# Performance work log

Measured on AMD Instinct MI355X. Metric: run time of the kernel, lower is better.

The kernel has to match this reference:

```python
import jax, jax.numpy as jnp
import numpy as np

B, S, H = 4, 2048, 1024
NH, HD = 16, 64
LN_EPS = 1e-5


def _l2norm(x, axis=-1, eps=1e-12):
    n = jnp.sqrt(jnp.sum(x * x, axis=axis, keepdims=True))
    return x / jnp.maximum(n, eps)


def setup_inputs() -> dict:
    key = jax.random.key(0)
    ks = jax.random.split(key, 10)
    sd = 0.02
    x = jax.random.normal(ks[0], (B, S, H), jnp.float32)
    Wq = jax.random.normal(ks[1], (H, H), jnp.float32) * sd
    Wk = jax.random.normal(ks[2], (H, H), jnp.float32) * sd
    Wv = jax.random.normal(ks[3], (H, H), jnp.float32) * sd
    Wa = jax.random.normal(ks[4], (NH, H), jnp.float32) * sd
    ba = jnp.zeros((NH,), jnp.float32)
    Wb = jax.random.normal(ks[5], (NH, H), jnp.float32) * sd
    bb = jnp.zeros((NH,), jnp.float32)
    Wg = jax.random.normal(ks[6], (H, H), jnp.float32) * sd
    Wo = jax.random.normal(ks[7], (H, H), jnp.float32) * sd
    ln_g = jnp.ones((H,), jnp.float32)
    ln_b = jnp.zeros((H,), jnp.float32)
    return {"x": x, "Wq": Wq, "Wk": Wk, "Wv": Wv, "Wa": Wa, "ba": ba,
            "Wb": Wb, "bb": bb, "Wg": Wg, "Wo": Wo, "ln_g": ln_g, "ln_b": ln_b}


def _forward(x, Wq, Wk, Wv, Wa, ba, Wb, bb, Wg, Wo, ln_g, ln_b):
    q = _l2norm((x @ Wq.T).reshape(B, S, NH, HD))  # [B,S,nh,hd]
    k = _l2norm((x @ Wk.T).reshape(B, S, NH, HD))
    v = jax.nn.silu(x @ Wv.T).reshape(B, S, NH, HD)
    alpha = jax.nn.sigmoid(x @ Wa.T + ba)  # [B,S,nh]
    beta = jax.nn.sigmoid(x @ Wb.T + bb)   # [B,S,nh]

    def step(state, inp):
        a_t, b_t, k_t, v_t, q_t = inp  # a,b: [B,nh]; k,v,q: [B,nh,hd]
        a_ = a_t[:, :, None, None]
        b_ = b_t[:, :, None, None]
        kk = k_t[..., :, None] * k_t[..., None, :]  # [B,nh,hd,hd]
        state = a_ * state * (1.0 - b_ * kk) + b_ * (v_t[..., :, None] * k_t[..., None, :])
        out_t = jnp.sum(state * q_t[..., None, :], axis=-1)  # [B,nh,hd]
        return state, out_t

    # time-major xs for scan
    xs = (jnp.moveaxis(alpha, 1, 0), jnp.moveaxis(beta, 1, 0),
          jnp.moveaxis(k, 1, 0), jnp.moveaxis(v, 1, 0), jnp.moveaxis(q, 1, 0))
    state0 = jnp.zeros((B, NH, HD, HD), x.dtype)
    _, outs = jax.lax.scan(step, state0, xs)  # [S,B,nh,hd]
    out = jnp.moveaxis(outs, 0, 1).reshape(B, S, H)

    # LayerNorm over total_dim
    mu = jnp.mean(out, axis=-1, keepdims=True)
    var = jnp.var(out, axis=-1, keepdims=True)
    out = (out - mu) / jnp.sqrt(var + LN_EPS) * ln_g + ln_b

    out = out * jax.nn.silu(x @ Wg.T)
    return out @ Wo.T


def reference(x, Wq, Wk, Wv, Wa, ba, Wb, bb, Wg, Wo, ln_g, ln_b):
    return _forward(x, Wq, Wk, Wv, Wa, ba, Wb, bb, Wg, Wo, ln_g, ln_b)
```

## Files before the change

kernel.cpp:

```cpp
#include <hip/hip_runtime.h>

typedef unsigned short u16;
typedef __bf16 bf16x8 __attribute__((ext_vector_type(8)));
typedef float f32x4 __attribute__((ext_vector_type(4)));

constexpr int Bq  = 4;
constexpr int Sq  = 2048;
constexpr int Hq  = 1024;
constexpr int NHq = 16;
constexpr int HDq = 64;
constexpr int CCH = 16;
constexpr int LCH = 128;

constexpr size_t OFF_WB = 0;
constexpr size_t OFF_XB = 10485760;
constexpr size_t OFF_Q  = 27262976;
constexpr size_t OFF_K  = 60817408;
constexpr size_t OFF_V  = 94371840;
constexpr size_t OFF_G  = 127926272;
constexpr size_t OFF_AL = 161480704;
constexpr size_t OFF_BE = 162004992;
constexpr size_t OFF_P  = 162529280;
constexpr size_t OFF_O  = 179306496;

__device__ __forceinline__ u16 f2bf(float f) {
  unsigned u = __float_as_uint(f);
  u += 0x7fffu + ((u >> 16) & 1u);
  return (u16)(u >> 16);
}
__device__ __forceinline__ float sigmoidf_(float x) { return 1.f / (1.f + __expf(-x)); }

__device__ __forceinline__ void async16(const void* g, void* l) {
  __builtin_amdgcn_global_load_lds((const __attribute__((address_space(1))) void*)g,
                                   (__attribute__((address_space(3))) void*)l, 16, 0, 0);
}

__global__ __launch_bounds__(256) void cvt_x_kernel(const float* __restrict__ in, u16* __restrict__ outp) {
  const size_t i = ((size_t)blockIdx.x * 256 + threadIdx.x) * 4;
  float4 f = *(const float4*)(in + i);
  ushort4 u; u.x = f2bf(f.x); u.y = f2bf(f.y); u.z = f2bf(f.z); u.w = f2bf(f.w);
  *(ushort4*)(outp + i) = u;
}

__global__ __launch_bounds__(256) void cvt_w_kernel(const float* __restrict__ w0, const float* __restrict__ w1,
    const float* __restrict__ w2, const float* __restrict__ w3, const float* __restrict__ w4,
    u16* __restrict__ outp) {
  const int z = blockIdx.z;
  const float* src = (z == 0) ? w0 : (z == 1) ? w1 : (z == 2) ? w2 : (z == 3) ? w3 : w4;
  const size_t i = ((size_t)blockIdx.x * 256 + threadIdx.x) * 4;
  float4 f = *(const float4*)(src + i);
  ushort4 u; u.x = f2bf(f.x); u.y = f2bf(f.y); u.z = f2bf(f.z); u.w = f2bf(f.w);
  *(ushort4*)(outp + (size_t)z * (1024 * 1024) + i) = u;
}

__global__ __launch_bounds__(256) void cvt_ab_kernel(const float* __restrict__ Wa, const float* __restrict__ Wb,
    u16* __restrict__ outp) {
  const size_t i = ((size_t)blockIdx.x * 256 + threadIdx.x) * 4;
  const int row = (int)(i >> 10);
  ushort4 u;
  if (row < 32) {
    const float* src = (row < 16) ? (Wa + i) : (Wb + i - 16 * 1024);
    float4 f = *(const float4*)src;
    u.x = f2bf(f.x); u.y = f2bf(f.y); u.z = f2bf(f.z); u.w = f2bf(f.w);
  } else {
    u.x = u.y = u.z = u.w = 0;
  }
  *(ushort4*)(outp + i) = u;
}


__device__ __forceinline__ void lda4(bf16x8 af[4][2], const u16* LA, int wr, int mh, int l15, int qd, int l7) {
#pragma unroll
  for (int i = 0; i < 4; ++i)
#pragma unroll
    for (int kk = 0; kk < 2; ++kk)
      af[i][kk] = *(const bf16x8*)(LA + (wr * 128 + mh * 64 + i * 16 + l15) * 64 + (((kk * 4 + qd) ^ l7) * 8));
}
__device__ __forceinline__ void ldb2(bf16x8 bf[2][2], const u16* LB, int wc, int nh, int l15, int qd, int l7) {
#pragma unroll
  for (int j = 0; j < 2; ++j)
#pragma unroll
    for (int kk = 0; kk < 2; ++kk)
      bf[j][kk] = *(const bf16x8*)(LB + (wc * 64 + nh * 32 + j * 16 + l15) * 64 + (((kk * 4 + qd) ^ l7) * 8));
}
__device__ __forceinline__ void mm16(f32x4 acc[8][4], const bf16x8 af[4][2], const bf16x8 bf[2][2], int mh, int nh) {
#pragma unroll
  for (int i = 0; i < 4; ++i)
#pragma unroll
    for (int j = 0; j < 2; ++j) {
      f32x4 c = acc[mh * 4 + i][nh * 2 + j];
      c = __builtin_amdgcn_mfma_f32_16x16x32_bf16(af[i][0], bf[j][0], c, 0, 0, 0);
      c = __builtin_amdgcn_mfma_f32_16x16x32_bf16(af[i][1], bf[j][1], c, 0, 0, 0);
      acc[mh * 4 + i][nh * 2 + j] = c;
    }
}
__device__ __forceinline__ void stageH(u16* LD, int bufp, int mat, int h, const u16* gRow0, int kElem,
                                       int rr, int sl8, int wv) {
  const u16* s0 = gRow0 + (size_t)(h * 128 + rr) * 1024 + kElem + sl8;
  u16* d = LD + bufp * 32768 + mat * 16384 + h * 8192 + wv * 512;
  async16(s0, d);
  async16(s0 + (size_t)(64 * 1024), d + 4096);
}

template<int S1, int S2, int VM>
__device__ __forceinline__ void tile16(u16* LD, int bp, int kt,
    const u16* gA, const u16* gB, f32x4 acc[8][4], bf16x8 af[4][2], bf16x8 bf0[2][2], bf16x8 bf1[2][2],
    int wr, int wc, int l15, int qd, int l7, int rr, int sl8, int wv) {
  const u16* LA = LD + bp * 32768;
  const u16* LB = LA + 16384;
  lda4(af, LA, wr, 0, l15, qd, l7);
  ldb2(bf0, LB, wc, 0, l15, qd, l7);
  if (S1) stageH(LD, bp ^ 1, 0, 0, gA, (kt + 1) * 64, rr, sl8, wv);
  __builtin_amdgcn_s_barrier();
  asm volatile("s_waitcnt lgkmcnt(0)" ::: "memory");
  __builtin_amdgcn_sched_barrier(0);
  __builtin_amdgcn_s_setprio(1);
  mm16(acc, af, bf0, 0, 0);
  __builtin_amdgcn_s_setprio(0);
  __builtin_amdgcn_s_barrier();
  ldb2(bf1, LB, wc, 1, l15, qd, l7);
  if (S1) stageH(LD, bp ^ 1, 0, 1, gA, (kt + 1) * 64, rr, sl8, wv);
  __builtin_amdgcn_s_barrier();
  asm volatile("s_waitcnt lgkmcnt(0)" ::: "memory");
  __builtin_amdgcn_sched_barrier(0);
  __builtin_amdgcn_s_setprio(1);
  mm16(acc, af, bf1, 0, 1);
  __builtin_amdgcn_s_setprio(0);
  __builtin_amdgcn_s_barrier();
  lda4(af, LA, wr, 1, l15, qd, l7);
  if (S2) stageH(LD, bp, 1, 0, gB, (kt + 2) * 64, rr, sl8, wv);
  __builtin_amdgcn_s_barrier();
  asm volatile("s_waitcnt lgkmcnt(0)" ::: "memory");
  __builtin_amdgcn_sched_barrier(0);
  __builtin_amdgcn_s_setprio(1);
  mm16(acc, af, bf0, 1, 0);
  __builtin_amdgcn_s_setprio(0);
  __builtin_amdgcn_s_barrier();
  if (S2) stageH(LD, bp, 1, 1, gB, (kt + 2) * 64, rr, sl8, wv);
  __builtin_amdgcn_s_barrier();
  __builtin_amdgcn_sched_barrier(0);
  __builtin_amdgcn_s_setprio(1);
  mm16(acc, af, bf1, 1, 1);
  __builtin_amdgcn_s_setprio(0);
  if (VM == 4) asm volatile("s_waitcnt vmcnt(4)" ::: "memory");
  else if (VM == 0) asm volatile("s_waitcnt vmcnt(0)" ::: "memory");
  __builtin_amdgcn_s_barrier();
}

__global__ __launch_bounds__(512, 2) void gemm256(const u16* __restrict__ A, const u16* __restrict__ Wall,
    const u16* __restrict__ Wab,
    float* __restrict__ Cq, float* __restrict__ Ck, float* __restrict__ Cv, float* __restrict__ Cg,
    float* __restrict__ al, float* __restrict__ be,
    const float* __restrict__ ba, const float* __restrict__ bb, int mode) {
  __shared__ __align__(16) u16 Lds[65536];
  u16* LD = &Lds[0];
  const int tid = threadIdx.x;
  const int wv = tid >> 6, lane = tid & 63;
  const int l15 = lane & 15, qd = lane >> 4, l7 = l15 & 7;
  const int wr = wv >> 2, wc = wv & 3;
  const int rr = tid >> 3, sl8 = ((tid & 7) ^ (rr & 7)) * 8;

  int mx, ny, z;
  const u16* Wm;
  if (mode == 0) { mx = blockIdx.x & 31; ny = blockIdx.x >> 5; z = 0; Wm = Wall; }
  else if (blockIdx.x < 32) { mx = blockIdx.x; ny = 0; z = 4; Wm = Wab; }
  else {
    const int b = blockIdx.x - 32;
    mx = b & 31; ny = (b >> 5) & 3; z = b >> 7;
    Wm = Wall + (size_t)z * (1024 * 1024);
  }
  const int m0 = mx * 256, n0 = ny * 256;
  const u16* gA = A + (size_t)m0 * 1024;
  const u16* gB = Wm + (size_t)n0 * 1024;

  f32x4 acc[8][4] = {};
  bf16x8 af[4][2], bf0[2][2], bf1[2][2];

  stageH(LD, 0, 0, 0, gA, 0,  rr, sl8, wv);
  stageH(LD, 0, 0, 1, gA, 0,  rr, sl8, wv);
  stageH(LD, 0, 1, 0, gB, 0,  rr, sl8, wv);
  stageH(LD, 0, 1, 1, gB, 0,  rr, sl8, wv);
  stageH(LD, 1, 1, 0, gB, 64, rr, sl8, wv);
  stageH(LD, 1, 1, 1, gB, 64, rr, sl8, wv);
  asm volatile("s_waitcnt vmcnt(4)" ::: "memory");
  __builtin_amdgcn_s_barrier();

#pragma unroll 1
  for (int t2 = 0; t2 < 7; ++t2) {
    tile16<1, 1, 4>(LD, 0, 2 * t2,     gA, gB, acc, af, bf0, bf1, wr, wc, l15, qd, l7, rr, sl8, wv);
    tile16<1, 1, 4>(LD, 1, 2 * t2 + 1, gA, gB, acc, af, bf0, bf1, wr, wc, l15, qd, l7, rr, sl8, wv);
  }
  tile16<1, 0, 0>(LD, 0, 14, gA, gB, acc, af, bf0, bf1, wr, wc, l15, qd, l7, rr, sl8, wv);
  tile16<0, 0, -1>(LD, 1, 15, gA, gB, acc, af, bf0, bf1, wr, wc, l15, qd, l7, rr, sl8, wv);

  if (mode == 1 && z == 4) {
    if (wc == 0) {
      const float bav = ba[l15], bbv = bb[l15];
#pragma unroll
      for (int mi = 0; mi < 8; ++mi) {
        const int row = m0 + wr * 128 + mi * 16 + qd * 4;
#pragma unroll
        for (int r = 0; r < 4; ++r) {
          al[(size_t)(row + r) * 16 + l15] = sigmoidf_(acc[mi][0][r] + bav);
          be[(size_t)(row + r) * 16 + l15] = sigmoidf_(acc[mi][1][r] + bbv);
        }
      }
    }
    return;
  }
  if (mode == 1 && z <= 1) {
#pragma unroll
    for (int mi = 0; mi < 8; ++mi)
#pragma unroll
      for (int r = 0; r < 4; ++r) {
        float ss = acc[mi][0][r] * acc[mi][0][r] + acc[mi][1][r] * acc[mi][1][r]
                 + acc[mi][2][r] * acc[mi][2][r] + acc[mi][3][r] * acc[mi][3][r];
        ss += __shfl_xor(ss, 1); ss += __shfl_xor(ss, 2);
        ss += __shfl_xor(ss, 4); ss += __shfl_xor(ss, 8);
        const float rn = 1.f / fmaxf(sqrtf(ss), 1e-12f);
        acc[mi][0][r] *= rn; acc[mi][1][r] *= rn; acc[mi][2][r] *= rn; acc[mi][3][r] *= rn;
      }
  } else if (mode == 1 && z == 2) {
#pragma unroll
    for (int mi = 0; mi < 8; ++mi)
#pragma unroll
      for (int ni = 0; ni < 4; ++ni)
#pragma unroll
        for (int r = 0; r < 4; ++r)
          acc[mi][ni][r] = acc[mi][ni][r] * sigmoidf_(acc[mi][ni][r]);
  }
  float* C = (mode == 0) ? Cq : ((z == 0) ? Cq : (z == 1) ? Ck : (z == 2) ? Cv : Cg);
#pragma unroll
  for (int mi = 0; mi < 8; ++mi) {
    const int row = m0 + wr * 128 + mi * 16 + qd * 4;
#pragma unroll
    for (int ni = 0; ni < 4; ++ni) {
      const int col = n0 + wc * 64 + ni * 16 + l15;
#pragma unroll
      for (int r = 0; r < 4; ++r)
        C[(size_t)(row + r) * 1024 + col] = acc[mi][ni][r];
    }
  }
}

struct ScanLds1 { float kb[2][2][16 * 64]; float vb[2][2][16 * 64]; float ab[2][2][32]; };
struct ScanLds2 { float kb[2][2][16 * 64]; float qb[2][2][16 * 64]; float vb[2][2][16 * 64]; float ab[2][2][32]; };

__global__ __launch_bounds__(256, 2) void scan_p1(const float* __restrict__ k, const float* __restrict__ v,
    const float* __restrict__ al, const float* __restrict__ be,
    float* __restrict__ P, float* __restrict__ Q) {
  __shared__ ScanLds1 L;
  const int tid = threadIdx.x, wv = tid >> 6, lane = tid & 63;
  const int bh = blockIdx.x >> 3, cp = blockIdx.x & 7;
  const int b = bh >> 4, h = bh & 15;
  const int cw = wv >> 1, half = wv & 1;
  const int c = cp * 2 + cw;
  const int rg = lane >> 3, cg = lane & 7;
  const int r0 = half * 32 + rg * 4, c8 = cg * 8;
  const size_t base0[2] = { ((size_t)(b * Sq + (cp * 2 + 0) * LCH)) * 1024 + h * 64,
                            ((size_t)(b * Sq + (cp * 2 + 1) * LCH)) * 1024 + h * 64 };
  const size_t ab0[2]   = { ((size_t)(b * Sq + (cp * 2 + 0) * LCH)) * 16 + h,
                            ((size_t)(b * Sq + (cp * 2 + 1) * LCH)) * 16 + h };
  const int tokw = lane >> 4, seg = lane & 15;
  auto stage = [&](int tile, int bi) {
    #pragma unroll
    for (int j = 0; j < 4; ++j) {
      const int job = wv * 4 + j;
      const int ch = job >> 3, rem = job & 7, arr = rem >> 2, i = rem & 3;
      const float* src = arr ? v : k;
      float* dst = arr ? &L.vb[bi][ch][i * 256] : &L.kb[bi][ch][i * 256];
      async16(src + base0[ch] + (size_t)(tile * 16 + i * 4 + tokw) * 1024 + seg * 4, dst);
    }
    if (wv == 0) {
      const int ch = lane >> 5, w16 = (lane >> 4) & 1, tt = lane & 15;
      const float* s = w16 ? be : al;
      L.ab[bi][ch][w16 * 16 + tt] = s[ab0[ch] + (size_t)(tile * 16 + tt) * 16];
    }
  };
  float Pr[32], Qr[32];
  #pragma unroll
  for (int i = 0; i < 32; ++i) { Pr[i] = 1.f; Qr[i] = 0.f; }
  stage(0, 0);
  for (int tile = 0; tile < 8; ++tile) {
    __syncthreads();
    if (tile < 7) stage(tile + 1, (tile + 1) & 1);
    const int bi = tile & 1;
    const float* kbp = L.kb[bi][cw];
    const float* vbp = L.vb[bi][cw];
    const float* abp = L.ab[bi][cw];
    #pragma unroll 2
    for (int tt = 0; tt < 16; ++tt) {
      const float a = abp[tt], bt = abp[16 + tt];
      float4 kcv0 = *(const float4*)(kbp + tt * 64 + c8);
      float4 kcv1 = *(const float4*)(kbp + tt * 64 + c8 + 4);
      float4 krvv = *(const float4*)(kbp + tt * 64 + r0);
      float4 vrvv = *(const float4*)(vbp + tt * 64 + r0);
      const float kcv[8] = {kcv0.x, kcv0.y, kcv0.z, kcv0.w, kcv1.x, kcv1.y, kcv1.z, kcv1.w};
      const float krv[4] = {krvv.x, krvv.y, krvv.z, krvv.w};
      const float vrv[4] = {vrvv.x, vrvv.y, vrvv.z, vrvv.w};
      const float abt = a * bt;
      float c1[4], c2[4];
      #pragma unroll
      for (int i = 0; i < 4; ++i) { c1[i] = abt * krv[i]; c2[i] = bt * vrv[i]; }
      #pragma unroll
      for (int i = 0; i < 4; ++i)
        #pragma unroll
        for (int j = 0; j < 8; ++j) {
          const int e = i * 8 + j;
          const float A = fmaf(-c1[i], kcv[j], a);
          Qr[e] = fmaf(A, Qr[e], c2[i] * kcv[j]);
          Pr[e] *= A;
        }
    }
  }
  const size_t pbase = ((size_t)bh * CCH + c) * 4096 + (size_t)c8;
  #pragma unroll
  for (int i = 0; i < 4; ++i) {
    const size_t pi = pbase + (size_t)(r0 + i) * 64;
    *(float4*)(P + pi) = make_float4(Pr[i*8],   Pr[i*8+1], Pr[i*8+2], Pr[i*8+3]);
    *(float4*)(P + pi + 4) = make_float4(Pr[i*8+4], Pr[i*8+5], Pr[i*8+6], Pr[i*8+7]);
    *(float4*)(Q + pi) = make_float4(Qr[i*8],   Qr[i*8+1], Qr[i*8+2], Qr[i*8+3]);
    *(float4*)(Q + pi + 4) = make_float4(Qr[i*8+4], Qr[i*8+5], Qr[i*8+6], Qr[i*8+7]);
  }
}

__global__ __launch_bounds__(256) void scan_comb(float* __restrict__ P, const float* __restrict__ Q) {
  const int g = blockIdx.x * 256 + threadIdx.x;
  const int elem = g & 4095;
  const int bh = g >> 12;
  float s = 0.f;
  for (int c = 0; c < CCH; ++c) {
    const size_t idx = ((size_t)bh * CCH + c) * 4096 + elem;
    const float p = P[idx], qq = Q[idx];
    P[idx] = s;
    s = fmaf(p, s, qq);
  }
}

__global__ __launch_bounds__(256, 2) void scan_p2(const float* __restrict__ q, const float* __restrict__ k,
    const float* __restrict__ v, const float* __restrict__ al, const float* __restrict__ be,
    const float* __restrict__ Pini, float* __restrict__ o) {
  __shared__ ScanLds2 L;
  const int tid = threadIdx.x, wv = tid >> 6, lane = tid & 63;
  const int bh = blockIdx.x >> 3, cp = blockIdx.x & 7;
  const int b = bh >> 4, h = bh & 15;
  const int cw = wv >> 1, half = wv & 1;
  const int c = cp * 2 + cw;
  const int rg = lane >> 3, cg = lane & 7;
  const int r0 = half * 32 + rg * 4, c8 = cg * 8;
  const size_t base0[2] = { ((size_t)(b * Sq + (cp * 2 + 0) * LCH)) * 1024 + h * 64,
                            ((size_t)(b * Sq + (cp * 2 + 1) * LCH)) * 1024 + h * 64 };
  const size_t ab0[2]   = { ((size_t)(b * Sq + (cp * 2 + 0) * LCH)) * 16 + h,
                            ((size_t)(b * Sq + (cp * 2 + 1) * LCH)) * 16 + h };
  const size_t mybase = base0[cw];
  const size_t pbase = ((size_t)bh * CCH + c) * 4096 + (size_t)c8;
  const int tokw = lane >> 4, seg = lane & 15;
  auto stage = [&](int tile, int bi) {
    #pragma unroll
    for (int j = 0; j < 6; ++j) {
      const int job = wv * 6 + j;
      const int ch = job / 12, rem = job % 12, arr = rem >> 2, i = rem & 3;
      const float* src = (arr == 0) ? k : (arr == 1) ? q : v;
      float* dst = (arr == 0) ? &L.kb[bi][ch][i * 256] : (arr == 1) ? &L.qb[bi][ch][i * 256]
                                                                    : &L.vb[bi][ch][i * 256];
      async16(src + base0[ch] + (size_t)(tile * 16 + i * 4 + tokw) * 1024 + seg * 4, dst);
    }
    if (wv == 0) {
      const int ch = lane >> 5, w16 = (lane >> 4) & 1, tt = lane & 15;
      const float* s = w16 ? be : al;
      L.ab[bi][ch][w16 * 16 + tt] = s[ab0[ch] + (size_t)(tile * 16 + tt) * 16];
    }
  };
  float st[32];
  #pragma unroll
  for (int i = 0; i < 4; ++i) {
    float4 s0 = *(const float4*)(Pini + pbase + (size_t)(r0 + i) * 64);
    float4 s1 = *(const float4*)(Pini + pbase + (size_t)(r0 + i) * 64 + 4);
    st[i*8]   = s0.x; st[i*8+1] = s0.y; st[i*8+2] = s0.z; st[i*8+3] = s0.w;
    st[i*8+4] = s1.x; st[i*8+5] = s1.y; st[i*8+6] = s1.z; st[i*8+7] = s1.w;
  }
  stage(0, 0);
  const bool hi4 = (cg & 4), hi2 = (cg & 2);
  const int rowIdx = r0 + (cg >> 1);
  const bool doStore = ((cg & 1) == 0);
  for (int tile = 0; tile < 8; ++tile) {
    __syncthreads();
    if (tile < 7) stage(tile + 1, (tile + 1) & 1);
    const int bi = tile & 1;
    const float* kbp = L.kb[bi][cw];
    const float* qbp = L.qb[bi][cw];
    const float* vbp = L.vb[bi][cw];
    const float* abp = L.ab[bi][cw];
    #pragma unroll 2
    for (int tt = 0; tt < 16; ++tt) {
      const int t = tile * 16 + tt;
      const float a = abp[tt], bt = abp[16 + tt];
      float4 kcv0 = *(const float4*)(kbp + tt * 64 + c8);
      float4 kcv1 = *(const float4*)(kbp + tt * 64 + c8 + 4);
      float4 qcv0 = *(const float4*)(qbp + tt * 64 + c8);
      float4 qcv1 = *(const float4*)(qbp + tt * 64 + c8 + 4);
      float4 krvv = *(const float4*)(kbp + tt * 64 + r0);
      float4 vrvv = *(const float4*)(vbp + tt * 64 + r0);
      const float kcv[8] = {kcv0.x, kcv0.y, kcv0.z, kcv0.w, kcv1.x, kcv1.y, kcv1.z, kcv1.w};
      const float qcv[8] = {qcv0.x, qcv0.y, qcv0.z, qcv0.w, qcv1.x, qcv1.y, qcv1.z, qcv1.w};
      const float krv[4] = {krvv.x, krvv.y, krvv.z, krvv.w};
      const float vrv[4] = {vrvv.x, vrvv.y, vrvv.z, vrvv.w};
      const float abt = a * bt;
      float c1[4], c2[4];
      #pragma unroll
      for (int i = 0; i < 4; ++i) { c1[i] = abt * krv[i]; c2[i] = bt * vrv[i]; }
      float p[4];
      #pragma unroll
      for (int i = 0; i < 4; ++i) p[i] = 0.f;
      #pragma unroll
      for (int i = 0; i < 4; ++i)
        #pragma unroll
        for (int j = 0; j < 8; ++j) {
          const int e = i * 8 + j;
          const float A = fmaf(-c1[i], kcv[j], a);
          st[e] = fmaf(A, st[e], c2[i] * kcv[j]);
          p[i] = fmaf(st[e], qcv[j], p[i]);
        }
      float r2[2];
      #pragma unroll
      for (int i = 0; i < 2; ++i) {
        const float send = hi4 ? p[i] : p[i + 2];
        const float recv = __shfl_xor(send, 4);
        r2[i] = (hi4 ? p[i + 2] : p[i]) + recv;
      }
      float r1;
      {
        const float send = hi2 ? r2[0] : r2[1];
        const float recv = __shfl_xor(send, 2);
        r1 = (hi2 ? r2[1] : r2[0]) + recv;
      }
      const float tot = r1 + __shfl_xor(r1, 1);
      if (doStore) o[mybase + (size_t)t * 1024 + rowIdx] = tot;
    }
  }
}

__global__ __launch_bounds__(256) void ln_gate_kernel(const float* __restrict__ o, const float* __restrict__ g,
    const float* __restrict__ ln_g, const float* __restrict__ ln_b, u16* __restrict__ y) {
  const int t = blockIdx.x, tid = threadIdx.x;
  const size_t row = (size_t)t * 1024;
  float4 xv = *(const float4*)(o + row + tid * 4);
  float s  = xv.x + xv.y + xv.z + xv.w;
  float s2 = xv.x * xv.x + xv.y * xv.y + xv.z * xv.z + xv.w * xv.w;
  #pragma unroll
  for (int m = 1; m < 64; m <<= 1) { s += __shfl_xor(s, m); s2 += __shfl_xor(s2, m); }
  __shared__ float red[8];
  const int w = tid >> 6, lane = tid & 63;
  if (lane == 0) { red[w] = s; red[4 + w] = s2; }
  __syncthreads();
  s  = red[0] + red[1] + red[2] + red[3];
  s2 = red[4] + red[5] + red[6] + red[7];
  const float mu = s * (1.f / 1024.f);
  const float var = s2 * (1.f / 1024.f) - mu * mu;
  const float rstd = rsqrtf(var + 1e-5f);
  float4 gv = *(const float4*)(g + row + tid * 4);
  float4 lg = *(const float4*)(ln_g + tid * 4);
  float4 lb = *(const float4*)(ln_b + tid * 4);
  ushort4 u;
  u.x = f2bf(((xv.x - mu) * rstd * lg.x + lb.x) * (gv.x * sigmoidf_(gv.x)));
  u.y = f2bf(((xv.y - mu) * rstd * lg.y + lb.y) * (gv.y * sigmoidf_(gv.y)));
  u.z = f2bf(((xv.z - mu) * rstd * lg.z + lb.z) * (gv.z * sigmoidf_(gv.z)));
  u.w = f2bf(((xv.w - mu) * rstd * lg.w + lb.w) * (gv.w * sigmoidf_(gv.w)));
  *(ushort4*)(y + row + tid * 4) = u;
}

extern "C" void kernel_launch(void* const* d_in, const int* in_sizes, int n_in,
                              void* d_out, int out_size, void* d_ws, size_t ws_size,
                              hipStream_t stream) {
  const float* x    = (const float*)d_in[0];
  const float* Wq   = (const float*)d_in[1];
  const float* Wk   = (const float*)d_in[2];
  const float* Wv   = (const float*)d_in[3];
  const float* Wa   = (const float*)d_in[4];
  const float* ba   = (const float*)d_in[5];
  const float* Wb   = (const float*)d_in[6];
  const float* bb   = (const float*)d_in[7];
  const float* Wg   = (const float*)d_in[8];
  const float* Wo   = (const float*)d_in[9];
  const float* ln_g = (const float*)d_in[10];
  const float* ln_b = (const float*)d_in[11];
  float* out = (float*)d_out;
  char* ws = (char*)d_ws;

  u16*   wb  = (u16*)(ws + OFF_WB);
  u16*   xb  = (u16*)(ws + OFF_XB);
  float* qf  = (float*)(ws + OFF_Q);
  float* kf  = (float*)(ws + OFF_K);
  float* vf  = (float*)(ws + OFF_V);
  float* gf  = (float*)(ws + OFF_G);
  float* al  = (float*)(ws + OFF_AL);
  float* be  = (float*)(ws + OFF_BE);
  u16*   wab = (u16*)(ws + OFF_P);
  float* Pb  = (float*)(ws + OFF_P);
  float* Qc  = (float*)(ws + OFF_XB);
  float* of  = (float*)(ws + OFF_O);
  u16*   yb  = xb;

  cvt_x_kernel<<<8192, 256, 0, stream>>>(x, xb);
  cvt_w_kernel<<<dim3(1024, 1, 5), 256, 0, stream>>>(Wq, Wk, Wv, Wg, Wo, wb);
  cvt_ab_kernel<<<256, 256, 0, stream>>>(Wa, Wb, wab);
  gemm256<<<544, 512, 0, stream>>>(xb, wb, wab, qf, kf, vf, gf, al, be, ba, bb, 1);
  scan_p1<<<512, 256, 0, stream>>>(kf, vf, al, be, Pb, Qc);
  scan_comb<<<1024, 256, 0, stream>>>(Pb, Qc);
  scan_p2<<<512, 256, 0, stream>>>(qf, kf, vf, al, be, Pb, of);
  ln_gate_kernel<<<8192, 256, 0, stream>>>(of, gf, ln_g, ln_b, yb);
  gemm256<<<128, 512, 0, stream>>>(yb, wb + (size_t)4 * 1024 * 1024, wab,
                                   out, out, out, out, al, be, ba, bb, 0);
}
```

Before: 425.7 us.

## Map one scan chunk per block with four waves splitting state rows

The chunked scan kernels now give each 256-thread block a single chunk, and each wave owns 16 state rows instead of two waves sharing 32 rows. This halves the per-thread state registers (32 to 16), doubles the grid to 1024 blocks, and raises launch bounds to 4 blocks per CU. The goal is more parallelism and occupancy for the latency-bound recurrence. In exchange, k and q column vectors are reloaded from LDS by more waves per state element, and the output reduction is rewritten with one fewer shuffle level.

Result: faster. 409.6 us (-3.8%).

```diff
diff --git a/kernel.cpp b/kernel.cpp
--- a/kernel.cpp
+++ b/kernel.cpp
@@ -243,67 +243,63 @@
   }
 }
 
-struct ScanLds1 { float kb[2][2][16 * 64]; float vb[2][2][16 * 64]; float ab[2][2][32]; };
-struct ScanLds2 { float kb[2][2][16 * 64]; float qb[2][2][16 * 64]; float vb[2][2][16 * 64]; float ab[2][2][32]; };
-
-__global__ __launch_bounds__(256, 2) void scan_p1(const float* __restrict__ k, const float* __restrict__ v,
+struct ScanLds1 { float kb[2][16 * 64]; float vb[2][16 * 64]; float ab[2][32]; };
+struct ScanLds2 { float kb[2][16 * 64]; float qb[2][16 * 64]; float vb[2][16 * 64]; float ab[2][32]; };
+
+__global__ __launch_bounds__(256, 4) void scan_p1(const float* __restrict__ k, const float* __restrict__ v,
     const float* __restrict__ al, const float* __restrict__ be,
     float* __restrict__ P, float* __restrict__ Q) {
   __shared__ ScanLds1 L;
   const int tid = threadIdx.x, wv = tid >> 6, lane = tid & 63;
-  const int bh = blockIdx.x >> 3, cp = blockIdx.x & 7;
+  const int bh = blockIdx.x >> 4, c = blockIdx.x & 15;
   const int b = bh >> 4, h = bh & 15;
-  const int cw = wv >> 1, half = wv & 1;
-  const int c = cp * 2 + cw;
   const int rg = lane >> 3, cg = lane & 7;
-  const int r0 = half * 32 + rg * 4, c8 = cg * 8;
-  const size_t base0[2] = { ((size_t)(b * Sq + (cp * 2 + 0) * LCH)) * 1024 + h * 64,
-                            ((size_t)(b * Sq + (cp * 2 + 1) * LCH)) * 1024 + h * 64 };
-  const size_t ab0[2]   = { ((size_t)(b * Sq + (cp * 2 + 0) * LCH)) * 16 + h,
-                            ((size_t)(b * Sq + (cp * 2 + 1) * LCH)) * 16 + h };
+  const int r0 = wv * 16 + rg * 2, c8 = cg * 8;
+  const size_t base0 = ((size_t)(b * Sq + c * LCH)) * 1024 + h * 64;
+  const size_t ab0   = ((size_t)(b * Sq + c * LCH)) * 16 + h;
   const int tokw = lane >> 4, seg = lane & 15;
   auto stage = [&](int tile, int bi) {
     #pragma unroll
-    for (int j = 0; j < 4; ++j) {
-      const int job = wv * 4 + j;
-      const int ch = job >> 3, rem = job & 7, arr = rem >> 2, i = rem & 3;
+    for (int j = 0; j < 2; ++j) {
+      const int job = wv * 2 + j;
+      const int arr = job >> 2, i = job & 3;
       const float* src = arr ? v : k;
-      float* dst = arr ? &L.vb[bi][ch][i * 256] : &L.kb[bi][ch][i * 256];
-      async16(src + base0[ch] + (size_t)(tile * 16 + i * 4 + tokw) * 1024 + seg * 4, dst);
-    }
-    if (wv == 0) {
-      const int ch = lane >> 5, w16 = (lane >> 4) & 1, tt = lane & 15;
+      float* dst = arr ? &L.vb[bi][i * 256] : &L.kb[bi][i * 256];
+      async16(src + base0 + (size_t)(tile * 16 + i * 4 + tokw) * 1024 + seg * 4, dst);
+    }
+    if (wv == 0 && lane < 32) {
+      const int w16 = lane >> 4, tt = lane & 15;
       const float* s = w16 ? be : al;
-      L.ab[bi][ch][w16 * 16 + tt] = s[ab0[ch] + (size_t)(tile * 16 + tt) * 16];
+      L.ab[bi][w16 * 16 + tt] = s[ab0 + (size_t)(tile * 16 + tt) * 16];
     }
   };
-  float Pr[32], Qr[32];
+  float Pr[16], Qr[16];
   #pragma unroll
-  for (int i = 0; i < 32; ++i) { Pr[i] = 1.f; Qr[i] = 0.f; }
+  for (int i = 0; i < 16; ++i) { Pr[i] = 1.f; Qr[i] = 0.f; }
   stage(0, 0);
   for (int tile = 0; tile < 8; ++tile) {
     __syncthreads();
     if (tile < 7) stage(tile + 1, (tile + 1) & 1);
     const int bi = tile & 1;
-    const float* kbp = L.kb[bi][cw];
-    const float* vbp = L.vb[bi][cw];
-    const float* abp = L.ab[bi][cw];
+    const float* kbp = L.kb[bi];
+    const float* vbp = L.vb[bi];
+    const float* abp = L.ab[bi];
     #pragma unroll 2
     for (int tt = 0; tt < 16; ++tt) {
       const float a = abp[tt], bt = abp[16 + tt];
       float4 kcv0 = *(const float4*)(kbp + tt * 64 + c8);
       float4 kcv1 = *(const float4*)(kbp + tt * 64 + c8 + 4);
-      float4 krvv = *(const float4*)(kbp + tt * 64 + r0);
-      float4 vrvv = *(const float4*)(vbp + tt * 64 + r0);
+      float2 krvv = *(const float2*)(kbp + tt * 64 + r0);
+      float2 vrvv = *(const float2*)(vbp + tt * 64 + r0);
       const float kcv[8] = {kcv0.x, kcv0.y, kcv0.z, kcv0.w, kcv1.x, kcv1.y, kcv1.z, kcv1.w};
-      const float krv[4] = {krvv.x, krvv.y, krvv.z, krvv.w};
-      const float vrv[4] = {vrvv.x, vrvv.y, vrvv.z, vrvv.w};
+      const float krv[2] = {krvv.x, krvv.y};
+      const float vrv[2] = {vrvv.x, vrvv.y};
       const float abt = a * bt;
-      float c1[4], c2[4];
+      float c1[2], c2[2];
       #pragma unroll
-      for (int i = 0; i < 4; ++i) { c1[i] = abt * krv[i]; c2[i] = bt * vrv[i]; }
+      for (int i = 0; i < 2; ++i) { c1[i] = abt * krv[i]; c2[i] = bt * vrv[i]; }
       #pragma unroll
-      for (int i = 0; i < 4; ++i)
+      for (int i = 0; i < 2; ++i)
         #pragma unroll
         for (int j = 0; j < 8; ++j) {
           const int e = i * 8 + j;
@@ -315,11 +311,11 @@
   }
   const size_t pbase = ((size_t)bh * CCH + c) * 4096 + (size_t)c8;
   #pragma unroll
-  for (int i = 0; i < 4; ++i) {
+  for (int i = 0; i < 2; ++i) {
     const size_t pi = pbase + (size_t)(r0 + i) * 64;
-    *(float4*)(P + pi) = make_float4(Pr[i*8],   Pr[i*8+1], Pr[i*8+2], Pr[i*8+3]);
+    *(float4*)(P + pi)     = make_float4(Pr[i*8],   Pr[i*8+1], Pr[i*8+2], Pr[i*8+3]);
     *(float4*)(P + pi + 4) = make_float4(Pr[i*8+4], Pr[i*8+5], Pr[i*8+6], Pr[i*8+7]);
-    *(float4*)(Q + pi) = make_float4(Qr[i*8],   Qr[i*8+1], Qr[i*8+2], Qr[i*8+3]);
+    *(float4*)(Q + pi)     = make_float4(Qr[i*8],   Qr[i*8+1], Qr[i*8+2], Qr[i*8+3]);
     *(float4*)(Q + pi + 4) = make_float4(Qr[i*8+4], Qr[i*8+5], Qr[i*8+6], Qr[i*8+7]);
   }
 }
@@ -337,60 +333,55 @@
   }
 }
 
-__global__ __launch_bounds__(256, 2) void scan_p2(const float* __restrict__ q, const float* __restrict__ k,
+__global__ __launch_bounds__(256, 4) void scan_p2(const float* __restrict__ q, const float* __restrict__ k,
     const float* __restrict__ v, const float* __restrict__ al, const float* __restrict__ be,
     const float* __restrict__ Pini, float* __restrict__ o) {
   __shared__ ScanLds2 L;
   const int tid = threadIdx.x, wv = tid >> 6, lane = tid & 63;
-  const int bh = blockIdx.x >> 3, cp = blockIdx.x & 7;
+  const int bh = blockIdx.x >> 4, c = blockIdx.x & 15;
   const int b = bh >> 4, h = bh & 15;
-  const int cw = wv >> 1, half = wv & 1;
-  const int c = cp * 2 + cw;
   const int rg = lane >> 3, cg = lane & 7;
-  const int r0 = half * 32 + rg * 4, c8 = cg * 8;
-  const size_t base0[2] = { ((size_t)(b * Sq + (cp * 2 + 0) * LCH)) * 1024 + h * 64,
-                            ((size_t)(b * Sq + (cp * 2 + 1) * LCH)) * 1024 + h * 64 };
-  const size_t ab0[2]   = { ((size_t)(b * Sq + (cp * 2 + 0) * LCH)) * 16 + h,
-                            ((size_t)(b * Sq + (cp * 2 + 1) * LCH)) * 16 + h };
-  const size_t mybase = base0[cw];
+  const int r0 = wv * 16 + rg * 2, c8 = cg * 8;
+  const size_t base0 = ((size_t)(b * Sq + c * LCH)) * 1024 + h * 64;
+  const size_t ab0   = ((size_t)(b * Sq + c * LCH)) * 16 + h;
   const size_t pbase = ((size_t)bh * CCH + c) * 4096 + (size_t)c8;
   const int tokw = lane >> 4, seg = lane & 15;
   auto stage = [&](int tile, int bi) {
     #pragma unroll
-    for (int j = 0; j < 6; ++j) {
-      const int job = wv * 6 + j;
-      const int ch = job / 12, rem = job % 12, arr = rem >> 2, i = rem & 3;
+    for (int j = 0; j < 3; ++j) {
+      const int job = wv * 3 + j;
+      const int arr = job >> 2, i = job & 3;
       const float* src = (arr == 0) ? k : (arr == 1) ? q : v;
-      float* dst = (arr == 0) ? &L.kb[bi][ch][i * 256] : (arr == 1) ? &L.qb[bi][ch][i * 256]
-                                                                    : &L.vb[bi][ch][i * 256];
-      async16(src + base0[ch] + (size_t)(tile * 16 + i * 4 + tokw) * 1024 + seg * 4, dst);
-    }
-    if (wv == 0) {
-      const int ch = lane >> 5, w16 = (lane >> 4) & 1, tt = lane & 15;
+      float* dst = (arr == 0) ? &L.kb[bi][i * 256] : (arr == 1) ? &L.qb[bi][i * 256]
+                                                                : &L.vb[bi][i * 256];
+      async16(src + base0 + (size_t)(tile * 16 + i * 4 + tokw) * 1024 + seg * 4, dst);
+    }
+    if (wv == 0 && lane < 32) {
+      const int w16 = lane >> 4, tt = lane & 15;
       const float* s = w16 ? be : al;
-      L.ab[bi][ch][w16 * 16 + tt] = s[ab0[ch] + (size_t)(tile * 16 + tt) * 16];
+      L.ab[bi][w16 * 16 + tt] = s[ab0 + (size_t)(tile * 16 + tt) * 16];
     }
   };
-  float st[32];
+  float st[16];
   #pragma unroll
-  for (int i = 0; i < 4; ++i) {
+  for (int i = 0; i < 2; ++i) {
     float4 s0 = *(const float4*)(Pini + pbase + (size_t)(r0 + i) * 64);
     float4 s1 = *(const float4*)(Pini + pbase + (size_t)(r0 + i) * 64 + 4);
     st[i*8]   = s0.x; st[i*8+1] = s0.y; st[i*8+2] = s0.z; st[i*8+3] = s0.w;
     st[i*8+4] = s1.x; st[i*8+5] = s1.y; st[i*8+6] = s1.z; st[i*8+7] = s1.w;
   }
   stage(0, 0);
-  const bool hi4 = (cg & 4), hi2 = (cg & 2);
-  const int rowIdx = r0 + (cg >> 1);
-  const bool doStore = ((cg & 1) == 0);
+  const bool hi4 = (cg & 4);
+  const int rowIdx = r0 + (cg >> 2);
+  const bool doStore = ((cg & 3) == 0);
   for (int tile = 0; tile < 8; ++tile) {
     __syncthreads();
     if (tile < 7) stage(tile + 1, (tile + 1) & 1);
     const int bi = tile & 1;
-    const float* kbp = L.kb[bi][cw];
-    const float* qbp = L.qb[bi][cw];
-    const float* vbp = L.vb[bi][cw];
-    const float* abp = L.ab[bi][cw];
+    const float* kbp = L.kb[bi];
+    const float* qbp = L.qb[bi];
+    const float* vbp = L.vb[bi];
+    const float* abp = L.ab[bi];
     #pragma unroll 2
     for (int tt = 0; tt < 16; ++tt) {
       const int t = tile * 16 + tt;
@@ -399,21 +390,20 @@
       float4 kcv1 = *(const float4*)(kbp + tt * 64 + c8 + 4);
       float4 qcv0 = *(const float4*)(qbp + tt * 64 + c8);
       float4 qcv1 = *(const float4*)(qbp + tt * 64 + c8 + 4);
-      float4 krvv = *(const float4*)(kbp + tt * 64 + r0);
-      float4 vrvv = *(const float4*)(vbp + tt * 64 + r0);
+      float2 krvv = *(const float2*)(kbp + tt * 64 + r0);
+      float2 vrvv = *(const float2*)(vbp + tt * 64 + r0);
       const float kcv[8] = {kcv0.x, kcv0.y, kcv0.z, kcv0.w, kcv1.x, kcv1.y, kcv1.z, kcv1.w};
       const float qcv[8] = {qcv0.x, qcv0.y, qcv0.z, qcv0.w, qcv1.x, qcv1.y, qcv1.z, qcv1.w};
-      const float krv[4] = {krvv.x, krvv.y, krvv.z, krvv.w};
-      const float vrv[4] = {vrvv.x, vrvv.y, vrvv.z, vrvv.w};
+      const float krv[2] = {krvv.x, krvv.y};
+      const float vrv[2] = {vrvv.x, vrvv.y};
       const float abt = a * bt;
-      float c1[4], c2[4];
+      float c1[2], c2[2];
       #pragma unroll
-      for (int i = 0; i < 4; ++i) { c1[i] = abt * krv[i]; c2[i] = bt * vrv[i]; }
-      float p[4];
+      for (int i = 0; i < 2; ++i) { c1[i] = abt * krv[i]; c2[i] = bt * vrv[i]; }
+      float p[2];
+      p[0] = 0.f; p[1] = 0.f;
       #pragma unroll
-      for (int i = 0; i < 4; ++i) p[i] = 0.f;
-      #pragma unroll
-      for (int i = 0; i < 4; ++i)
+      for (int i = 0; i < 2; ++i)
         #pragma unroll
         for (int j = 0; j < 8; ++j) {
           const int e = i * 8 + j;
@@ -421,21 +411,12 @@
           st[e] = fmaf(A, st[e], c2[i] * kcv[j]);
           p[i] = fmaf(st[e], qcv[j], p[i]);
         }
-      float r2[2];
-      #pragma unroll
-      for (int i = 0; i < 2; ++i) {
-        const float send = hi4 ? p[i] : p[i + 2];
-        const float recv = __shfl_xor(send, 4);
-        r2[i] = (hi4 ? p[i + 2] : p[i]) + recv;
-      }
-      float r1;
-      {
-        const float send = hi2 ? r2[0] : r2[1];
-        const float recv = __shfl_xor(send, 2);
-        r1 = (hi2 ? r2[1] : r2[0]) + recv;
-      }
-      const float tot = r1 + __shfl_xor(r1, 1);
-      if (doStore) o[mybase + (size_t)t * 1024 + rowIdx] = tot;
+      float my    = hi4 ? p[1] : p[0];
+      float other = hi4 ? p[0] : p[1];
+      my += __shfl_xor(other, 4);
+      my += __shfl_xor(my, 2);
+      my += __shfl_xor(my, 1);
+      if (doStore) o[base0 + (size_t)t * 1024 + rowIdx] = my;
     }
   }
 }
@@ -505,9 +486,9 @@
   cvt_w_kernel<<<dim3(1024, 1, 5), 256, 0, stream>>>(Wq, Wk, Wv, Wg, Wo, wb);
   cvt_ab_kernel<<<256, 256, 0, stream>>>(Wa, Wb, wab);
   gemm256<<<544, 512, 0, stream>>>(xb, wb, wab, qf, kf, vf, gf, al, be, ba, bb, 1);
-  scan_p1<<<512, 256, 0, stream>>>(kf, vf, al, be, Pb, Qc);
+  scan_p1<<<1024, 256, 0, stream>>>(kf, vf, al, be, Pb, Qc);
   scan_comb<<<1024, 256, 0, stream>>>(Pb, Qc);
-  scan_p2<<<512, 256, 0, stream>>>(qf, kf, vf, al, be, Pb, of);
+  scan_p2<<<1024, 256, 0, stream>>>(qf, kf, vf, al, be, Pb, of);
   ln_gate_kernel<<<8192, 256, 0, stream>>>(of, gf, ln_g, ln_b, yb);
   gemm256<<<128, 512, 0, stream>>>(yb, wb + (size_t)4 * 1024 * 1024, wab,
                                    out, out, out, out, al, be, ba, bb, 0);
```
